# Optimization experiments

Hardware: AMD Instinct MI355X
Metric: run time of the kernel (lower is better)

Reference implementation:

```python
import jax, jax.numpy as jnp
import numpy as np

N = 102400          # input_size (mesh nodes)
SFC = 2             # number of space-filling curves
K, S, P = 32, 4, 16 # kernel_size, stride, padding (= K//2)
OPADS = [1, 1, 1, 0]  # decoder output paddings per convT layer
NFC = 16            # num_final_channels
L0 = 401            # inv_conv_start
SIZE_FC = [12832, 1024, 128]
B = 64
# convT layer j: ConvTranspose1d(channels[-j] -> channels[-j-1]); channels=[1,8,16,16,16]
CONV_IO = [(16, 16), (16, 16), (16, 8), (8, 1)]


def conv_transpose1d(x, w, b, stride, padding, output_padding):
    # x: (B, Cin, L); w: torch layout (Cin, Cout, K)
    k = w.shape[-1]
    w_conv = jnp.flip(w, -1).transpose(1, 0, 2)  # (Cout, Cin, K)
    out = jax.lax.conv_general_dilated(
        x, w_conv, window_strides=(1,),
        padding=[(k - 1 - padding, k - 1 - padding + output_padding)],
        lhs_dilation=(stride,),
        dimension_numbers=('NCH', 'OIH', 'NCH'))
    return out + b[None, :, None]


def setup_inputs() -> dict:
    key = jax.random.key(0)
    ks = jax.random.split(key, 12)
    f32 = jnp.float32

    def nrm(k, shape, scale):
        return jax.random.normal(k, shape, f32) * scale

    # inverse SFC orderings: permutations of [0, N); plus/minus neighbours per repo helpers
    rng = np.random.RandomState(0)
    inv = np.stack([rng.permutation(N) for _ in range(SFC)]).astype(np.int32)
    plus = np.concatenate([inv[:, 1:], inv[:, -1:]], axis=1)   # find_plus_neigh
    minus = np.concatenate([inv[:, :1], inv[:, :-1]], axis=1)  # find_minus_neigh

    inp = {
        'x': nrm(ks[0], (B, SIZE_FC[2]), 1.0),
        'fc_w1': nrm(ks[1], (SIZE_FC[1], SIZE_FC[2]), 0.05),
        'fc_b1': jnp.full((SIZE_FC[1],), 0.001, f32),
        'fc_w2': nrm(ks[2], (SIZE_FC[0], SIZE_FC[1]), 0.02),
        'fc_b2': jnp.full((SIZE_FC[0],), 0.001, f32),
        'nn_w': jnp.full((SFC, N, 3), 1.0 / 3.0, f32) + nrm(ks[3], (SFC, N, 3), 0.01),
        'nn_b': jnp.zeros((SFC, N), f32),
        'ord_idx': jnp.asarray(inv),
        'minus_idx': jnp.asarray(minus),
        'plus_idx': jnp.asarray(plus),
    }
    for j, (cin, cout) in enumerate(CONV_IO):
        inp[f'conv_w{j+1}'] = nrm(ks[4 + j], (SFC, cin, cout, K), 0.03)
        inp[f'conv_b{j+1}'] = jnp.full((SFC, cout), 0.001, f32)
    return inp


def reference(x, fc_w1, fc_b1, fc_w2, fc_b2,
              conv_w1, conv_b1, conv_w2, conv_b2,
              conv_w3, conv_b3, conv_w4, conv_b4,
              nn_w, nn_b, ord_idx, minus_idx, plus_idx):
    act = jnp.tanh
    conv_ws = [conv_w1, conv_w2, conv_w3, conv_w4]
    conv_bs = [conv_b1, conv_b2, conv_b3, conv_b4]

    # FC stack (decoder walks size_fc in reverse)
    h = act(x @ fc_w1.T + fc_b1)
    h = act(h @ fc_w2.T + fc_b2)
    h = h.reshape(-1, SIZE_FC[0] // SFC, SFC)  # (B, split, sfc_nums)

    z = None
    for i in range(SFC):
        b = h[..., i].reshape(-1, NFC, L0)  # (B, 16, 401)
        for j in range(len(conv_ws)):
            b = act(conv_transpose1d(b, conv_ws[j][i], conv_bs[j][i], S, P, OPADS[j]))
        b = b.reshape(-1, N)  # (B, N)
        # SFC gather of (minus, self, plus) neighbours + NearestNeighbouring weighted sum
        tt = jnp.stack([b[:, minus_idx[i]], b[:, ord_idx[i]], b[:, plus_idx[i]]], axis=-1)  # (B, N, 3)
        z_i = act(jnp.einsum('bnm,nm->bn', tt, nn_w[i]) + nn_b[i])
        z = z_i if z is None else z + z_i
    return act(z)  # sfc_nums > 1: sum over curves then activate
```

## Files before the change

kernel.cpp:

```cpp
#include <hip/hip_runtime.h>

#define NNODES 102400

__device__ __forceinline__ float ftanh(float x) {
    float a = fabsf(x);
    float e = __expf(-2.0f * a);
    float t = (1.0f - e) / (1.0f + e);
    return copysignf(t, x);
}

__global__ __launch_bounds__(256) void fc1_kernel(
    const float* __restrict__ x, const float* __restrict__ w1,
    const float* __restrict__ b1, float* __restrict__ h1t)
{
    const int b = threadIdx.x & 63;
    const int o = blockIdx.x * 4 + __builtin_amdgcn_readfirstlane(threadIdx.x >> 6);
    const float* xr = x + b * 128;
    const float* wr = w1 + o * 128;
    float acc = 0.f;
#pragma unroll
    for (int k = 0; k < 128; ++k) acc = fmaf(xr[k], wr[k], acc);
    h1t[o * 64 + b] = ftanh(acc + b1[o]);
}

__global__ __launch_bounds__(128) void fc2_gemm_kernel(
    const float* __restrict__ h1t,
    const float* __restrict__ w2,
    float* __restrict__ part)
{
    __shared__ float Wl[32][68];
    __shared__ float Hl[64][64];
    const int t  = threadIdx.x;
    const int o0 = blockIdx.x * 32;
    const int ks = blockIdx.y;
    const int ob = (t >> 4) * 4;
    const int b4 = (t & 15) * 4;

    float acc[4][4] = {};
    const int kbase = ks * 256;
#pragma unroll 1
    for (int kt = 0; kt < 4; ++kt) {
        const int k0 = kbase + kt * 64;
        {
            const int row = t >> 2;
            const int c0  = (t & 3) * 4;
            const float* src = w2 + (size_t)(o0 + row) * 1024 + k0;
#pragma unroll
            for (int i = 0; i < 4; ++i) {
                const float4 v = *reinterpret_cast<const float4*>(src + c0 + 16 * i);
                *reinterpret_cast<float4*>(&Wl[row][c0 + 16 * i]) = v;
            }
        }
        {
            const float* src = h1t + (size_t)k0 * 64;
            float* dst = &Hl[0][0];
#pragma unroll
            for (int i = 0; i < 8; ++i) {
                const int f4 = t + 128 * i;
                const float4 v = *reinterpret_cast<const float4*>(src + f4 * 4);
                *reinterpret_cast<float4*>(dst + f4 * 4) = v;
            }
        }
        __syncthreads();
#pragma unroll
        for (int kk = 0; kk < 16; ++kk) {
            const int k4 = kk * 4;
            float wv[4][4], hv[4][4];
#pragma unroll
            for (int i = 0; i < 4; ++i) {
                const float4 v = *reinterpret_cast<const float4*>(&Wl[ob + i][k4]);
                wv[i][0] = v.x; wv[i][1] = v.y; wv[i][2] = v.z; wv[i][3] = v.w;
            }
#pragma unroll
            for (int j = 0; j < 4; ++j) {
                const float4 v = *reinterpret_cast<const float4*>(&Hl[k4 + j][b4]);
                hv[j][0] = v.x; hv[j][1] = v.y; hv[j][2] = v.z; hv[j][3] = v.w;
            }
#pragma unroll
            for (int i = 0; i < 4; ++i)
#pragma unroll
                for (int j = 0; j < 4; ++j)
#pragma unroll
                    for (int jb = 0; jb < 4; ++jb)
                        acc[i][jb] = fmaf(wv[i][j], hv[j][jb], acc[i][jb]);
        }
        __syncthreads();
    }
    float* pb = part + ((size_t)ks * 12832 + o0) * 64;
#pragma unroll
    for (int i = 0; i < 4; ++i) {
        const float4 v = make_float4(acc[i][0], acc[i][1], acc[i][2], acc[i][3]);
        *reinterpret_cast<float4*>(pb + (size_t)(ob + i) * 64 + b4) = v;
    }
}

__global__ __launch_bounds__(256) void fc2_reduce_kernel(
    const float* __restrict__ part, const float* __restrict__ b2,
    float* __restrict__ h2t)
{
    const int idx = blockIdx.x * 256 + threadIdx.x;
    const int o = idx >> 6;
    const float s = part[idx] + part[821248 + idx]
                  + part[1642496 + idx] + part[2463744 + idx];
    h2t[idx] = ftanh(s + b2[o]);
}

__device__ __forceinline__ void pack_one(const float* __restrict__ w, float* __restrict__ wp,
                                         int CIN, int COUT, int idx)
{
    const int k = idx & 31;
    int r = idx >> 5;
    const int co = r % COUT; r /= COUT;
    const int ci = r % CIN;
    const int i  = r / CIN;
    const int k0 = k & 3, d = k >> 2;
    wp[(((i * 4 + k0) * 8 + d) * CIN + ci) * COUT + co] = w[idx];
}

__global__ __launch_bounds__(256) void pack_all_kernel(
    const float* __restrict__ w1, const float* __restrict__ w2,
    const float* __restrict__ w3, const float* __restrict__ w4,
    float* __restrict__ wp1, float* __restrict__ wp2,
    float* __restrict__ wp3, float* __restrict__ wp4)
{
    const int idx = blockIdx.x * 256 + threadIdx.x;
    if (idx < 16384)       pack_one(w1, wp1, 16, 16, idx);
    else if (idx < 32768)  pack_one(w2, wp2, 16, 16, idx - 16384);
    else if (idx < 40960)  pack_one(w3, wp3, 16,  8, idx - 32768);
    else if (idx < 41472)  pack_one(w4, wp4,  8,  1, idx - 40960);
}

template<int CIN, int COUT, int TT, int COG>
__global__ __launch_bounds__(256, 4) void convt3_kernel(
    const float* __restrict__ x, size_t sfc_xstride, int cistride, int jstride,
    const float* __restrict__ wp, int sfc_wstride,
    const float* __restrict__ bias, int sfc_bstride,
    float* __restrict__ y, size_t sfc_ystride,
    int Lin, int Lout)
{
    constexpr int CPG = COUT / COG;
    const int b = threadIdx.x & 63;
    const int widx = __builtin_amdgcn_readfirstlane(threadIdx.x >> 6);
    const int t0 = blockIdx.x * (4 * TT) + widx;
    if (t0 >= Lout) return;
    const int cb = blockIdx.z * CPG;
    const int k0   = (t0 + 16) & 3;
    const int jhi0 = (t0 + 16) >> 2;
    constexpr int NJ = TT + 7;
    const float* xs = x + (size_t)blockIdx.y * sfc_xstride + b;
    const float* wk = wp + blockIdx.y * sfc_wstride + k0 * (8 * CIN * COUT) + cb;
    const float* bs = bias + blockIdx.y * sfc_bstride + cb;

    float acc[TT][CPG];
#pragma unroll
    for (int co = 0; co < CPG; ++co) {
        const float bv = bs[co];
#pragma unroll
        for (int tt = 0; tt < TT; ++tt) acc[tt][co] = bv;
    }

    for (int ci = 0; ci < CIN; ++ci) {
        const float* xpc = xs + (size_t)ci * cistride;
        float xv[NJ];
#pragma unroll
        for (int q = 0; q < NJ; ++q) {
            const int j = jhi0 - 7 + q;
            xv[q] = (j >= 0 && j < Lin) ? xpc[(size_t)j * jstride] : 0.f;
        }
        const float* wc = wk + ci * COUT;
#pragma unroll
        for (int d = 0; d < 8; ++d) {
            const float* wd = wc + d * CIN * COUT;
            float wv[CPG];
            if constexpr ((CPG & 3) == 0) {
#pragma unroll
                for (int cq = 0; cq < CPG; cq += 4) {
                    const float4 w4 = *reinterpret_cast<const float4*>(wd + cq);
                    wv[cq + 0] = w4.x; wv[cq + 1] = w4.y;
                    wv[cq + 2] = w4.z; wv[cq + 3] = w4.w;
                }
            } else {
#pragma unroll
                for (int co = 0; co < CPG; ++co) wv[co] = wd[co];
            }
#pragma unroll
            for (int tt = 0; tt < TT; ++tt) {
                const float xx = xv[7 + tt - d];
#pragma unroll
                for (int co = 0; co < CPG; ++co)
                    acc[tt][co] = fmaf(xx, wv[co], acc[tt][co]);
            }
        }
    }
#pragma unroll
    for (int tt = 0; tt < TT; ++tt) {
        const int t = t0 + 4 * tt;
        if (t < Lout) {
#pragma unroll
            for (int co = 0; co < CPG; ++co)
                y[(size_t)blockIdx.y * sfc_ystride + ((size_t)(cb + co) * Lout + t) * 64 + b] =
                    ftanh(acc[tt][co]);
        }
    }
}

__global__ __launch_bounds__(256) void final_kernel(
    const float* __restrict__ d0, const float* __restrict__ d1,
    const float* __restrict__ nn_w, const float* __restrict__ nn_b,
    const int* __restrict__ mi, const int* __restrict__ oi, const int* __restrict__ pi,
    float* __restrict__ out)
{
    const int b = threadIdx.x & 63;
    const int widx = __builtin_amdgcn_readfirstlane(threadIdx.x >> 6);
    const int n0 = blockIdx.x * 8 + widx * 2;
#pragma unroll
    for (int nn = 0; nn < 2; ++nn) {
        const int n = n0 + nn;
        float z = 0.f;
        {
            const int m = mi[n], o = oi[n], p = pi[n];
            const float* wv = nn_w + (size_t)n * 3;
            float v = wv[0] * d0[(size_t)m * 64 + b]
                    + wv[1] * d0[(size_t)o * 64 + b]
                    + wv[2] * d0[(size_t)p * 64 + b] + nn_b[n];
            z += ftanh(v);
        }
        {
            const int m = mi[NNODES + n], o = oi[NNODES + n], p = pi[NNODES + n];
            const float* wv = nn_w + (size_t)(NNODES + n) * 3;
            float v = wv[0] * d1[(size_t)m * 64 + b]
                    + wv[1] * d1[(size_t)o * 64 + b]
                    + wv[2] * d1[(size_t)p * 64 + b] + nn_b[NNODES + n];
            z += ftanh(v);
        }
        out[(size_t)b * NNODES + n] = ftanh(z);
    }
}

extern "C" void kernel_launch(void* const* d_in, const int* in_sizes, int n_in,
                              void* d_out, int out_size, void* d_ws, size_t ws_size,
                              hipStream_t stream)
{
    const float* x     = (const float*)d_in[0];
    const float* fc_w1 = (const float*)d_in[1];
    const float* fc_b1 = (const float*)d_in[2];
    const float* fc_w2 = (const float*)d_in[3];
    const float* fc_b2 = (const float*)d_in[4];
    const float* nn_w  = (const float*)d_in[5];
    const float* nn_b  = (const float*)d_in[6];
    const int* ord_i   = (const int*)d_in[7];
    const int* minus_i = (const int*)d_in[8];
    const int* plus_i  = (const int*)d_in[9];
    const float* conv_w1 = (const float*)d_in[10];
    const float* conv_b1 = (const float*)d_in[11];
    const float* conv_w2 = (const float*)d_in[12];
    const float* conv_b2 = (const float*)d_in[13];
    const float* conv_w3 = (const float*)d_in[14];
    const float* conv_b3 = (const float*)d_in[15];
    const float* conv_w4 = (const float*)d_in[16];
    const float* conv_b4 = (const float*)d_in[17];
    float* out = (float*)d_out;

    const size_t SZ_Y1 = (size_t)16 * 1601 * 64;
    const size_t SZ_Y2 = (size_t)16 * 6401 * 64;
    const size_t SZ_Y3 = (size_t)8  * 25601 * 64;
    const size_t SZ_Y4 = (size_t)NNODES * 64;

    const size_t need2 = ((size_t)65536 + 821248 + 2 * SZ_Y1 + 2 * SZ_Y2 + SZ_Y3 + 2 * SZ_Y4 + 41984) * 4;
    const int NS = (ws_size >= need2) ? 2 : 1;

    float* ws  = (float*)d_ws;
    float* h1t = ws;
    float* h2t = h1t + 65536;
    float* y1  = h2t + 821248;
    float* y2  = y1  + (size_t)NS * SZ_Y1;
    float* y3  = y2  + (size_t)NS * SZ_Y2;
    float* y4  = y3  + SZ_Y3;
    float* wp1 = y4  + 2 * SZ_Y4;
    float* wp2 = wp1 + 16384;
    float* wp3 = wp2 + 16384;
    float* wp4 = wp3 + 8192;
    float* part = y3;

    fc1_kernel<<<dim3(256),  dim3(256), 0, stream>>>(x, fc_w1, fc_b1, h1t);
    fc2_gemm_kernel<<<dim3(401, 4), dim3(128), 0, stream>>>(h1t, fc_w2, part);
    fc2_reduce_kernel<<<dim3(3208), dim3(256), 0, stream>>>(part, fc_b2, h2t);
    pack_all_kernel<<<dim3(162), dim3(256), 0, stream>>>(
        conv_w1, conv_w2, conv_w3, conv_w4, wp1, wp2, wp3, wp4);

    for (int s0 = 0; s0 < 2; s0 += NS) {
        convt3_kernel<16, 16, 1, 2><<<dim3(401, NS, 2), dim3(256), 0, stream>>>(
            h2t + s0 * 64, 64, 401 * 128, 128,
            wp1 + s0 * 8192, 8192, conv_b1 + s0 * 16, 16,
            y1, SZ_Y1, 401, 1601);
        convt3_kernel<16, 16, 4, 2><<<dim3(401, NS, 2), dim3(256), 0, stream>>>(
            y1, SZ_Y1, 1601 * 64, 64,
            wp2 + s0 * 8192, 8192, conv_b2 + s0 * 16, 16,
            y2, SZ_Y2, 1601, 6401);
        if (NS == 1) {
            convt3_kernel<16, 8, 6, 1><<<dim3(1067, 1, 1), dim3(256), 0, stream>>>(
                y2, 0, 6401 * 64, 64,
                wp3 + s0 * 4096, 0, conv_b3 + s0 * 8, 0,
                y3, 0, 6401, 25601);
            convt3_kernel<8, 1, 12, 1><<<dim3(2134, 1, 1), dim3(256), 0, stream>>>(
                y3, 0, 25601 * 64, 64,
                wp4 + s0 * 256, 0, conv_b4 + s0, 0,
                y4 + (size_t)s0 * SZ_Y4, 0, 25601, 102400);
        }
    }
    if (NS == 2) {
        for (int s = 0; s < 2; ++s) {
            convt3_kernel<16, 8, 6, 1><<<dim3(1067, 1, 1), dim3(256), 0, stream>>>(
                y2 + (size_t)s * SZ_Y2, 0, 6401 * 64, 64,
                wp3 + s * 4096, 0, conv_b3 + s * 8, 0,
                y3, 0, 6401, 25601);
            convt3_kernel<8, 1, 12, 1><<<dim3(2134, 1, 1), dim3(256), 0, stream>>>(
                y3, 0, 25601 * 64, 64,
                wp4 + s * 256, 0, conv_b4 + s, 0,
                y4 + (size_t)s * SZ_Y4, 0, 25601, 102400);
        }
    }

    final_kernel<<<dim3(12800), dim3(256), 0, stream>>>(
        y4, y4 + SZ_Y4, nn_w, nn_b, minus_i, ord_i, plus_i, out);
}
```

Measured before the change: 340.2 us.

## Batch both SFC curves in conv3/conv4, add unguarded interior path and register-weight conv4

Splits each transposed-convolution loop into an interior variant without bounds checks and a guarded edge variant. Adds a dedicated last-layer kernel that keeps its 8x8 weights in registers. Layer 3 now splits its output channels across two groups for more blocks. When the workspace is large enough, both curves of layers 3 and 4 run in single launches with separate y3 buffers. This cuts launch count and branch overhead and raises occupancy, at the cost of more workspace and duplicated code paths.

```diff
diff --git a/kernel.cpp b/kernel.cpp
--- a/kernel.cpp
+++ b/kernel.cpp
@@ -130,6 +130,50 @@
     else if (idx < 41472)  pack_one(w4, wp4,  8,  1, idx - 40960);
 }
 
+template<int CIN, int CPG, int TT, bool GUARD>
+__device__ __forceinline__ void conv_core(
+    const float* __restrict__ xs, int cistride, int jstride, int Lin,
+    const float* __restrict__ wk, int wco, int jhi0, float (&acc)[TT][CPG])
+{
+    constexpr int NJ = TT + 7;
+    for (int ci = 0; ci < CIN; ++ci) {
+        const float* xpc = xs + (size_t)ci * cistride;
+        float xv[NJ];
+#pragma unroll
+        for (int q = 0; q < NJ; ++q) {
+            const int j = jhi0 - 7 + q;
+            if constexpr (GUARD)
+                xv[q] = (j >= 0 && j < Lin) ? xpc[(size_t)j * jstride] : 0.f;
+            else
+                xv[q] = xpc[(size_t)j * jstride];
+        }
+        const float* wc = wk + ci * wco;
+#pragma unroll
+        for (int d = 0; d < 8; ++d) {
+            const float* wd = wc + d * CIN * wco;
+            float wv[CPG];
+            if constexpr ((CPG & 3) == 0) {
+#pragma unroll
+                for (int cq = 0; cq < CPG; cq += 4) {
+                    const float4 w4 = *reinterpret_cast<const float4*>(wd + cq);
+                    wv[cq + 0] = w4.x; wv[cq + 1] = w4.y;
+                    wv[cq + 2] = w4.z; wv[cq + 3] = w4.w;
+                }
+            } else {
+#pragma unroll
+                for (int co = 0; co < CPG; ++co) wv[co] = wd[co];
+            }
+#pragma unroll
+            for (int tt = 0; tt < TT; ++tt) {
+                const float xx = xv[7 + tt - d];
+#pragma unroll
+                for (int co = 0; co < CPG; ++co)
+                    acc[tt][co] = fmaf(xx, wv[co], acc[tt][co]);
+            }
+        }
+    }
+}
+
 template<int CIN, int COUT, int TT, int COG>
 __global__ __launch_bounds__(256, 4) void convt3_kernel(
     const float* __restrict__ x, size_t sfc_xstride, int cistride, int jstride,
@@ -146,7 +190,6 @@
     const int cb = blockIdx.z * CPG;
     const int k0   = (t0 + 16) & 3;
     const int jhi0 = (t0 + 16) >> 2;
-    constexpr int NJ = TT + 7;
     const float* xs = x + (size_t)blockIdx.y * sfc_xstride + b;
     const float* wk = wp + blockIdx.y * sfc_wstride + k0 * (8 * CIN * COUT) + cb;
     const float* bs = bias + blockIdx.y * sfc_bstride + cb;
@@ -159,48 +202,84 @@
         for (int tt = 0; tt < TT; ++tt) acc[tt][co] = bv;
     }
 
+    const bool interior = (jhi0 >= 7) && (jhi0 + TT - 1 < Lin);
+    if (interior)
+        conv_core<CIN, CPG, TT, false>(xs, cistride, jstride, Lin, wk, COUT, jhi0, acc);
+    else
+        conv_core<CIN, CPG, TT, true >(xs, cistride, jstride, Lin, wk, COUT, jhi0, acc);
+
+#pragma unroll
+    for (int tt = 0; tt < TT; ++tt) {
+        const int t = t0 + 4 * tt;
+        if (t < Lout) {
+#pragma unroll
+            for (int co = 0; co < CPG; ++co)
+                y[(size_t)blockIdx.y * sfc_ystride + ((size_t)(cb + co) * Lout + t) * 64 + b] =
+                    ftanh(acc[tt][co]);
+        }
+    }
+}
+
+template<int CIN, int TT, bool GUARD>
+__device__ __forceinline__ void conv4_core(
+    const float* __restrict__ xs, int cistride, int Lin, int jhi0,
+    const float (&wreg)[8][CIN], float (&acc)[TT])
+{
+    constexpr int NJ = TT + 7;
     for (int ci = 0; ci < CIN; ++ci) {
         const float* xpc = xs + (size_t)ci * cistride;
         float xv[NJ];
 #pragma unroll
         for (int q = 0; q < NJ; ++q) {
             const int j = jhi0 - 7 + q;
-            xv[q] = (j >= 0 && j < Lin) ? xpc[(size_t)j * jstride] : 0.f;
-        }
-        const float* wc = wk + ci * COUT;
-#pragma unroll
-        for (int d = 0; d < 8; ++d) {
-            const float* wd = wc + d * CIN * COUT;
-            float wv[CPG];
-            if constexpr ((CPG & 3) == 0) {
-#pragma unroll
-                for (int cq = 0; cq < CPG; cq += 4) {
-                    const float4 w4 = *reinterpret_cast<const float4*>(wd + cq);
-                    wv[cq + 0] = w4.x; wv[cq + 1] = w4.y;
-                    wv[cq + 2] = w4.z; wv[cq + 3] = w4.w;
-                }
-            } else {
-#pragma unroll
-                for (int co = 0; co < CPG; ++co) wv[co] = wd[co];
-            }
-#pragma unroll
-            for (int tt = 0; tt < TT; ++tt) {
-                const float xx = xv[7 + tt - d];
-#pragma unroll
-                for (int co = 0; co < CPG; ++co)
-                    acc[tt][co] = fmaf(xx, wv[co], acc[tt][co]);
-            }
-        }
-    }
+            if constexpr (GUARD)
+                xv[q] = (j >= 0 && j < Lin) ? xpc[(size_t)j * 64] : 0.f;
+            else
+                xv[q] = xpc[(size_t)j * 64];
+        }
+#pragma unroll
+        for (int d = 0; d < 8; ++d)
+#pragma unroll
+            for (int tt = 0; tt < TT; ++tt)
+                acc[tt] = fmaf(xv[7 + tt - d], wreg[d][ci], acc[tt]);
+    }
+}
+
+template<int CIN, int TT>
+__global__ __launch_bounds__(256, 3) void convt4_kernel(
+    const float* __restrict__ x, size_t sfc_xstride, int cistride,
+    const float* __restrict__ wp, int sfc_wstride,
+    const float* __restrict__ bias, int sfc_bstride,
+    float* __restrict__ y, size_t sfc_ystride, int Lin, int Lout)
+{
+    const int b = threadIdx.x & 63;
+    const int widx = __builtin_amdgcn_readfirstlane(threadIdx.x >> 6);
+    const int t0 = blockIdx.x * (4 * TT) + widx;
+    if (t0 >= Lout) return;
+    const int k0   = (t0 + 16) & 3;
+    const int jhi0 = (t0 + 16) >> 2;
+    const float* wk = wp + blockIdx.y * sfc_wstride + k0 * (8 * CIN);
+    float wreg[8][CIN];
+#pragma unroll
+    for (int d = 0; d < 8; ++d)
+#pragma unroll
+        for (int ci = 0; ci < CIN; ++ci)
+            wreg[d][ci] = wk[d * CIN + ci];
+    const float bv = bias[blockIdx.y * sfc_bstride];
+    float acc[TT];
+#pragma unroll
+    for (int tt = 0; tt < TT; ++tt) acc[tt] = bv;
+    const float* xs = x + (size_t)blockIdx.y * sfc_xstride + b;
+
+    const bool interior = (jhi0 >= 7) && (jhi0 + TT - 1 < Lin);
+    if (interior) conv4_core<CIN, TT, false>(xs, cistride, Lin, jhi0, wreg, acc);
+    else          conv4_core<CIN, TT, true >(xs, cistride, Lin, jhi0, wreg, acc);
+
+    float* yb = y + (size_t)blockIdx.y * sfc_ystride;
 #pragma unroll
     for (int tt = 0; tt < TT; ++tt) {
         const int t = t0 + 4 * tt;
-        if (t < Lout) {
-#pragma unroll
-            for (int co = 0; co < CPG; ++co)
-                y[(size_t)blockIdx.y * sfc_ystride + ((size_t)(cb + co) * Lout + t) * 64 + b] =
-                    ftanh(acc[tt][co]);
-        }
+        if (t < Lout) yb[(size_t)t * 64 + b] = ftanh(acc[tt]);
     }
 }
 
@@ -266,8 +345,11 @@
     const size_t SZ_Y3 = (size_t)8  * 25601 * 64;
     const size_t SZ_Y4 = (size_t)NNODES * 64;
 
-    const size_t need2 = ((size_t)65536 + 821248 + 2 * SZ_Y1 + 2 * SZ_Y2 + SZ_Y3 + 2 * SZ_Y4 + 41984) * 4;
-    const int NS = (ws_size >= need2) ? 2 : 1;
+    const size_t need22 = 56638976ull * 4;
+    const size_t need21 = 43531264ull * 4;
+    int NS = 1, NY3 = 1;
+    if (ws_size >= need22)      { NS = 2; NY3 = 2; }
+    else if (ws_size >= need21) { NS = 2; NY3 = 1; }
 
     float* ws  = (float*)d_ws;
     float* h1t = ws;
@@ -275,7 +357,7 @@
     float* y1  = h2t + 821248;
     float* y2  = y1  + (size_t)NS * SZ_Y1;
     float* y3  = y2  + (size_t)NS * SZ_Y2;
-    float* y4  = y3  + SZ_Y3;
+    float* y4  = y3  + (size_t)NY3 * SZ_Y3;
     float* wp1 = y4  + 2 * SZ_Y4;
     float* wp2 = wp1 + 16384;
     float* wp3 = wp2 + 16384;
@@ -297,28 +379,29 @@
             y1, SZ_Y1, 1601 * 64, 64,
             wp2 + s0 * 8192, 8192, conv_b2 + s0 * 16, 16,
             y2, SZ_Y2, 1601, 6401);
-        if (NS == 1) {
-            convt3_kernel<16, 8, 6, 1><<<dim3(1067, 1, 1), dim3(256), 0, stream>>>(
-                y2, 0, 6401 * 64, 64,
-                wp3 + s0 * 4096, 0, conv_b3 + s0 * 8, 0,
-                y3, 0, 6401, 25601);
-            convt3_kernel<8, 1, 12, 1><<<dim3(2134, 1, 1), dim3(256), 0, stream>>>(
-                y3, 0, 25601 * 64, 64,
-                wp4 + s0 * 256, 0, conv_b4 + s0, 0,
-                y4 + (size_t)s0 * SZ_Y4, 0, 25601, 102400);
-        }
-    }
-    if (NS == 2) {
-        for (int s = 0; s < 2; ++s) {
-            convt3_kernel<16, 8, 6, 1><<<dim3(1067, 1, 1), dim3(256), 0, stream>>>(
-                y2 + (size_t)s * SZ_Y2, 0, 6401 * 64, 64,
-                wp3 + s * 4096, 0, conv_b3 + s * 8, 0,
-                y3, 0, 6401, 25601);
-            convt3_kernel<8, 1, 12, 1><<<dim3(2134, 1, 1), dim3(256), 0, stream>>>(
-                y3, 0, 25601 * 64, 64,
-                wp4 + s * 256, 0, conv_b4 + s, 0,
-                y4 + (size_t)s * SZ_Y4, 0, 25601, 102400);
-        }
+        if (NY3 == 1) {
+            for (int s = s0; s < s0 + NS; ++s) {
+                const float* xin = y2 + (size_t)(NS == 2 ? (s - s0) : 0) * SZ_Y2;
+                convt3_kernel<16, 8, 6, 2><<<dim3(1067, 1, 2), dim3(256), 0, stream>>>(
+                    xin, 0, 6401 * 64, 64,
+                    wp3 + s * 4096, 0, conv_b3 + s * 8, 0,
+                    y3, 0, 6401, 25601);
+                convt4_kernel<8, 12><<<dim3(2134, 1), dim3(256), 0, stream>>>(
+                    y3, 0, 25601 * 64,
+                    wp4 + s * 256, 0, conv_b4 + s, 0,
+                    y4 + (size_t)s * SZ_Y4, 0, 25601, 102400);
+            }
+        }
+    }
+    if (NY3 == 2) {
+        convt3_kernel<16, 8, 6, 2><<<dim3(1067, 2, 2), dim3(256), 0, stream>>>(
+            y2, SZ_Y2, 6401 * 64, 64,
+            wp3, 4096, conv_b3, 8,
+            y3, SZ_Y3, 6401, 25601);
+        convt4_kernel<8, 12><<<dim3(2134, 2), dim3(256), 0, stream>>>(
+            y3, SZ_Y3, 25601 * 64,
+            wp4, 256, conv_b4, 1,
+            y4, SZ_Y4, 25601, 102400);
     }
 
     final_kernel<<<dim3(12800), dim3(256), 0, stream>>>(
```

New measurement: 301.1 us. 11.5% less time.
